# Optimization experiments

Measured on AMD Instinct MI355X. Metric: run time of the kernel, lower is better.

Reference implementation:

```python
import jax, jax.numpy as jnp
import numpy as np

D, P, R, K = 1024, 256, 64, 1024  # directions, sampling points, rank, subcarriers

def setup_inputs() -> dict:
    key = jax.random.key(0)
    k1, k2, k3 = jax.random.split(key, 3)
    return {
        "attenuation_vectors": jax.random.normal(k1, (D, P, R), dtype=jnp.float32),
        "radiation_vectors": jax.random.normal(k2, (D, P, R), dtype=jnp.float32),
        "frequency_basis_vectors": jax.random.normal(k3, (K, R), dtype=jnp.float32),
    }

def reference(attenuation_vectors, radiation_vectors, frequency_basis_vectors):
    # Original (per ray d, per subcarrier k):
    #   atten_factor[d,k] = sum_p sum_r u_rho[d,p,r] * F[k,r]
    #   rad_factor[d,k]   = sum_p sum_r u_s[d,p,r]   * F[k,r]
    #   csi[k] = (1/D) * sum_d atten_factor[d,k] * rad_factor[d,k]
    # Vectorized as two contractions over (p, r) plus a reduction over d.
    A = jnp.einsum('dpr,kr->dk', attenuation_vectors, frequency_basis_vectors)
    B = jnp.einsum('dpr,kr->dk', radiation_vectors, frequency_basis_vectors)
    num_directions = attenuation_vectors.shape[0]
    csi = jnp.sum(A * B, axis=0) / num_directions  # [K]
    return csi
```

## Files before the change

kernel.cpp:

```cpp
#include <hip/hip_runtime.h>

#define D_DIRS 1024
#define P_PTS  256
#define R_RANK 64
#define K_SUB  1024

typedef float v4f __attribute__((ext_vector_type(4)));

#define WS_A 0
#define WS_B (D_DIRS * R_RANK)
#define WS_M (2 * D_DIRS * R_RANK)
#define WS_MSUM 0
#define NB_B 32
#define DCHUNK (D_DIRS / NB_B)

__device__ __forceinline__ v4f ntload(const v4f* __restrict__ p) {
    return __builtin_nontemporal_load(p);
}

__device__ __forceinline__ v4f shfl_xor_v4(v4f v, int m) {
    v4f r;
    r.x = __shfl_xor(v.x, m);
    r.y = __shfl_xor(v.y, m);
    r.z = __shfl_xor(v.z, m);
    r.w = __shfl_xor(v.w, m);
    return r;
}

__global__ __launch_bounds__(512) void k_reduce_p(const float* __restrict__ atten,
                                                  const float* __restrict__ rad,
                                                  float* __restrict__ ws) {
    const int t    = threadIdx.x;
    const int wave = t >> 6;
    const int lane = t & 63;
    const int d    = blockIdx.x * 4 + (wave >> 1);
    const int half = wave & 1;
    const int r4g  = lane & 7;
    const int pr   = lane >> 3;

    const int base = pr * 16 + half * 8 + r4g;
    const v4f* A4 = (const v4f*)atten + (size_t)d * 4096 + base;
    const v4f* B4 = (const v4f*)rad   + (size_t)d * 4096 + base;

    v4f pa[8], pb[8], na[8], nb[8];
#pragma unroll
    for (int j = 0; j < 8; ++j) pa[j] = ntload(A4 + j * 128);
#pragma unroll
    for (int j = 0; j < 8; ++j) pb[j] = ntload(B4 + j * 128);

    v4f acc_a = {0.f, 0.f, 0.f, 0.f};
    v4f acc_b = {0.f, 0.f, 0.f, 0.f};

#pragma unroll
    for (int mc = 0; mc < 4; ++mc) {
        if (mc < 3) {
            const int off = (mc + 1) * 8 * 128;
#pragma unroll
            for (int j = 0; j < 8; ++j) na[j] = ntload(A4 + off + j * 128);
#pragma unroll
            for (int j = 0; j < 8; ++j) nb[j] = ntload(B4 + off + j * 128);
        }
        acc_a = acc_a + (((pa[0] + pa[1]) + (pa[2] + pa[3])) +
                         ((pa[4] + pa[5]) + (pa[6] + pa[7])));
        acc_b = acc_b + (((pb[0] + pb[1]) + (pb[2] + pb[3])) +
                         ((pb[4] + pb[5]) + (pb[6] + pb[7])));
#pragma unroll
        for (int j = 0; j < 8; ++j) { pa[j] = na[j]; pb[j] = nb[j]; }
    }

    acc_a = acc_a + shfl_xor_v4(acc_a, 8);
    acc_a = acc_a + shfl_xor_v4(acc_a, 16);
    acc_a = acc_a + shfl_xor_v4(acc_a, 32);
    acc_b = acc_b + shfl_xor_v4(acc_b, 8);
    acc_b = acc_b + shfl_xor_v4(acc_b, 16);
    acc_b = acc_b + shfl_xor_v4(acc_b, 32);

    if (pr == 0) {
        ((v4f*)(ws + WS_A))[d * 16 + half * 8 + r4g] = acc_a;
        ((v4f*)(ws + WS_B))[d * 16 + half * 8 + r4g] = acc_b;
    }
}

__global__ __launch_bounds__(256) void k_partial_m(float* __restrict__ ws) {
    const int bb = blockIdx.x;
    const int t  = threadIdx.x;

    __shared__ float sa[DCHUNK * R_RANK];
    __shared__ float sb[DCHUNK * R_RANK];

    const float4* a4 = (const float4*)(ws + WS_A) + bb * (DCHUNK * R_RANK / 4);
    const float4* b4 = (const float4*)(ws + WS_B) + bb * (DCHUNK * R_RANK / 4);
    float4* sa4 = (float4*)sa;
    float4* sb4 = (float4*)sb;
    sa4[t]       = a4[t];
    sa4[t + 256] = a4[t + 256];
    sb4[t]       = b4[t];
    sb4[t + 256] = b4[t + 256];
    __syncthreads();

    const int c  = t & 63;
    const int wg = t >> 6;

    float acc[16];
#pragma unroll
    for (int i = 0; i < 16; ++i) acc[i] = 0.f;

    for (int dd = 0; dd < DCHUNK; ++dd) {
        const float bv = sb[dd * 64 + c];
        const float4* ar = (const float4*)&sa[dd * 64 + wg * 16];
        const float4 a0 = ar[0], a1 = ar[1], a2 = ar[2], a3 = ar[3];
        acc[0]  += a0.x * bv; acc[1]  += a0.y * bv; acc[2]  += a0.z * bv; acc[3]  += a0.w * bv;
        acc[4]  += a1.x * bv; acc[5]  += a1.y * bv; acc[6]  += a1.z * bv; acc[7]  += a1.w * bv;
        acc[8]  += a2.x * bv; acc[9]  += a2.y * bv; acc[10] += a2.z * bv; acc[11] += a2.w * bv;
        acc[12] += a3.x * bv; acc[13] += a3.y * bv; acc[14] += a3.z * bv; acc[15] += a3.w * bv;
    }

    float* Mp = ws + WS_M + bb * 4096;
#pragma unroll
    for (int i = 0; i < 16; ++i) Mp[(wg * 16 + i) * 64 + c] = acc[i];
}

__global__ __launch_bounds__(256) void k_reduce_m(float* __restrict__ ws) {
    const int tg = blockIdx.x * 256 + threadIdx.x;
    const float4* Mp4 = (const float4*)(ws + WS_M);
    float4 s = make_float4(0.f, 0.f, 0.f, 0.f);
#pragma unroll
    for (int g = 0; g < NB_B; ++g) {
        const float4 v = Mp4[g * 1024 + tg];
        s.x += v.x; s.y += v.y; s.z += v.z; s.w += v.w;
    }
    ((float4*)(ws + WS_MSUM))[tg] = s;
}

__global__ __launch_bounds__(256) void k_csi(const float* __restrict__ ws,
                                             const float* __restrict__ freq,
                                             float* __restrict__ out) {
    const int bb = blockIdx.x;
    const int t  = threadIdx.x;

    __shared__ float Ms[64 * 68];
    __shared__ float Fs[64 * 65];
    __shared__ float red[4][64];

    const float4* M4 = (const float4*)(ws + WS_MSUM);
#pragma unroll
    for (int i = 0; i < 4; ++i) {
        const int idx4 = i * 256 + t;
        const float4 s = M4[idx4];
        const int r = idx4 >> 4, c4 = idx4 & 15;
        *(float4*)&Ms[r * 68 + c4 * 4] = s;
    }

    const float4* F4 = (const float4*)freq + bb * 1024;
#pragma unroll
    for (int i = 0; i < 4; ++i) {
        const int idx4 = i * 256 + t;
        const float4 v = F4[idx4];
        const int row = idx4 >> 4, c4 = idx4 & 15;
        Fs[row * 65 + c4 * 4 + 0] = v.x;
        Fs[row * 65 + c4 * 4 + 1] = v.y;
        Fs[row * 65 + c4 * 4 + 2] = v.z;
        Fs[row * 65 + c4 * 4 + 3] = v.w;
    }
    __syncthreads();

    const int kl = t & 63;
    const int jg = t >> 6;

    float h[16];
#pragma unroll
    for (int j = 0; j < 16; ++j) h[j] = 0.f;

    for (int r = 0; r < 64; ++r) {
        const float fv = Fs[kl * 65 + r];
        const float4* mr = (const float4*)&Ms[r * 68 + jg * 16];
        const float4 m0 = mr[0], m1 = mr[1], m2 = mr[2], m3 = mr[3];
        h[0]  += fv * m0.x; h[1]  += fv * m0.y; h[2]  += fv * m0.z; h[3]  += fv * m0.w;
        h[4]  += fv * m1.x; h[5]  += fv * m1.y; h[6]  += fv * m1.z; h[7]  += fv * m1.w;
        h[8]  += fv * m2.x; h[9]  += fv * m2.y; h[10] += fv * m2.z; h[11] += fv * m2.w;
        h[12] += fv * m3.x; h[13] += fv * m3.y; h[14] += fv * m3.z; h[15] += fv * m3.w;
    }

    float part = 0.f;
#pragma unroll
    for (int j = 0; j < 16; ++j) part += h[j] * Fs[kl * 65 + jg * 16 + j];

    red[jg][kl] = part;
    __syncthreads();
    if (t < 64) {
        out[bb * 64 + t] =
            (red[0][t] + red[1][t] + red[2][t] + red[3][t]) * (1.0f / (float)D_DIRS);
    }
}

extern "C" void kernel_launch(void* const* d_in, const int* in_sizes, int n_in,
                              void* d_out, int out_size, void* d_ws, size_t ws_size,
                              hipStream_t stream) {
    const float* atten = (const float*)d_in[0];
    const float* rad   = (const float*)d_in[1];
    const float* freq  = (const float*)d_in[2];
    float* out = (float*)d_out;
    float* ws  = (float*)d_ws;

    k_reduce_p<<<D_DIRS / 4, 512, 0, stream>>>(atten, rad, ws);
    k_partial_m<<<NB_B, 256, 0, stream>>>(ws);
    k_reduce_m<<<4, 256, 0, stream>>>(ws);
    k_csi<<<16, 256, 0, stream>>>(ws, freq, out);
}
```

Baseline: 149.4 us.

## Stream p-reduction inputs through LDS with async global_load_lds double buffering

The first kernel now reads attenuation and radiation data straight into LDS using global_load_lds, double-buffered across 16 chunks with manual waitcnt, instead of nontemporal register loads. Each wave now covers a contiguous half of the P dimension, so the per-direction partial sums are split into two halves in the workspace. The next kernel adds those halves together while staging its data into LDS. The aim is to raise the number of loads in flight and cut register pressure in this HBM-bound reduction. In exchange it adds LDS traffic and relies on hand-coded waitcnt values being correct.

```diff
diff --git a/kernel.cpp b/kernel.cpp
--- a/kernel.cpp
+++ b/kernel.cpp
@@ -1,4 +1,5 @@
 #include <hip/hip_runtime.h>
+#include <stdint.h>
 
 #define D_DIRS 1024
 #define P_PTS  256
@@ -7,16 +8,12 @@
 
 typedef float v4f __attribute__((ext_vector_type(4)));
 
-#define WS_A 0
-#define WS_B (D_DIRS * R_RANK)
-#define WS_M (2 * D_DIRS * R_RANK)
+#define WS_AP 0
+#define WS_BP (D_DIRS * 2 * R_RANK)
+#define WS_M  (2 * D_DIRS * 2 * R_RANK)
 #define WS_MSUM 0
 #define NB_B 32
 #define DCHUNK (D_DIRS / NB_B)
-
-__device__ __forceinline__ v4f ntload(const v4f* __restrict__ p) {
-    return __builtin_nontemporal_load(p);
-}
 
 __device__ __forceinline__ v4f shfl_xor_v4(v4f v, int m) {
     v4f r;
@@ -25,6 +22,12 @@
     r.z = __shfl_xor(v.z, m);
     r.w = __shfl_xor(v.w, m);
     return r;
+}
+
+__device__ __forceinline__ void load_lds_1k(const void* g, void* l) {
+    __builtin_amdgcn_global_load_lds(
+        (const __attribute__((address_space(1))) uint32_t*)g,
+        (__attribute__((address_space(3))) uint32_t*)l, 16, 0, 0);
 }
 
 __global__ __launch_bounds__(512) void k_reduce_p(const float* __restrict__ atten,
@@ -35,49 +38,58 @@
     const int lane = t & 63;
     const int d    = blockIdx.x * 4 + (wave >> 1);
     const int half = wave & 1;
-    const int r4g  = lane & 7;
-    const int pr   = lane >> 3;
-
-    const int base = pr * 16 + half * 8 + r4g;
-    const v4f* A4 = (const v4f*)atten + (size_t)d * 4096 + base;
-    const v4f* B4 = (const v4f*)rad   + (size_t)d * 4096 + base;
-
-    v4f pa[8], pb[8], na[8], nb[8];
-#pragma unroll
-    for (int j = 0; j < 8; ++j) pa[j] = ntload(A4 + j * 128);
-#pragma unroll
-    for (int j = 0; j < 8; ++j) pb[j] = ntload(B4 + j * 128);
+    const int rq   = lane & 15;
+    const int pg   = lane >> 4;
+
+    __shared__ char lds[8][2][2][2048];
+
+    const char* gA = (const char*)(atten + (size_t)d * 16384 + half * 8192);
+    const char* gB = (const char*)(rad   + (size_t)d * 16384 + half * 8192);
+    const int lane16 = lane * 16;
+
+    auto issue = [&](int c, int s) {
+        const char* ga = gA + c * 2048 + lane16;
+        const char* gb = gB + c * 2048 + lane16;
+        load_lds_1k(ga,        &lds[wave][0][s][0]);
+        load_lds_1k(ga + 1024, &lds[wave][0][s][1024]);
+        load_lds_1k(gb,        &lds[wave][1][s][0]);
+        load_lds_1k(gb + 1024, &lds[wave][1][s][1024]);
+    };
 
     v4f acc_a = {0.f, 0.f, 0.f, 0.f};
     v4f acc_b = {0.f, 0.f, 0.f, 0.f};
 
-#pragma unroll
-    for (int mc = 0; mc < 4; ++mc) {
-        if (mc < 3) {
-            const int off = (mc + 1) * 8 * 128;
-#pragma unroll
-            for (int j = 0; j < 8; ++j) na[j] = ntload(A4 + off + j * 128);
-#pragma unroll
-            for (int j = 0; j < 8; ++j) nb[j] = ntload(B4 + off + j * 128);
-        }
-        acc_a = acc_a + (((pa[0] + pa[1]) + (pa[2] + pa[3])) +
-                         ((pa[4] + pa[5]) + (pa[6] + pa[7])));
-        acc_b = acc_b + (((pb[0] + pb[1]) + (pb[2] + pb[3])) +
-                         ((pb[4] + pb[5]) + (pb[6] + pb[7])));
-#pragma unroll
-        for (int j = 0; j < 8; ++j) { pa[j] = na[j]; pb[j] = nb[j]; }
-    }
-
-    acc_a = acc_a + shfl_xor_v4(acc_a, 8);
+    auto consume = [&](int s) {
+        asm volatile("" ::: "memory");
+        const float* bufA = (const float*)&lds[wave][0][s][0];
+        const float* bufB = (const float*)&lds[wave][1][s][0];
+        const v4f a0 = *(const v4f*)(bufA + pg * 64 + rq * 4);
+        const v4f a1 = *(const v4f*)(bufA + (pg + 4) * 64 + rq * 4);
+        const v4f b0 = *(const v4f*)(bufB + pg * 64 + rq * 4);
+        const v4f b1 = *(const v4f*)(bufB + (pg + 4) * 64 + rq * 4);
+        acc_a = acc_a + (a0 + a1);
+        acc_b = acc_b + (b0 + b1);
+        asm volatile("" ::: "memory");
+    };
+
+    issue(0, 0);
+#pragma unroll
+    for (int c = 0; c < 15; ++c) {
+        issue(c + 1, (c + 1) & 1);
+        __builtin_amdgcn_s_waitcnt(0x0F74);
+        consume(c & 1);
+    }
+    __builtin_amdgcn_s_waitcnt(0x0F70);
+    consume(15 & 1);
+
     acc_a = acc_a + shfl_xor_v4(acc_a, 16);
     acc_a = acc_a + shfl_xor_v4(acc_a, 32);
-    acc_b = acc_b + shfl_xor_v4(acc_b, 8);
     acc_b = acc_b + shfl_xor_v4(acc_b, 16);
     acc_b = acc_b + shfl_xor_v4(acc_b, 32);
 
-    if (pr == 0) {
-        ((v4f*)(ws + WS_A))[d * 16 + half * 8 + r4g] = acc_a;
-        ((v4f*)(ws + WS_B))[d * 16 + half * 8 + r4g] = acc_b;
+    if (pg == 0) {
+        ((v4f*)(ws + WS_AP))[d * 32 + half * 16 + rq] = acc_a;
+        ((v4f*)(ws + WS_BP))[d * 32 + half * 16 + rq] = acc_b;
     }
 }
 
@@ -88,14 +100,18 @@
     __shared__ float sa[DCHUNK * R_RANK];
     __shared__ float sb[DCHUNK * R_RANK];
 
-    const float4* a4 = (const float4*)(ws + WS_A) + bb * (DCHUNK * R_RANK / 4);
-    const float4* b4 = (const float4*)(ws + WS_B) + bb * (DCHUNK * R_RANK / 4);
+    const float4* aP = (const float4*)(ws + WS_AP) + bb * (DCHUNK * 32);
+    const float4* bP = (const float4*)(ws + WS_BP) + bb * (DCHUNK * 32);
     float4* sa4 = (float4*)sa;
     float4* sb4 = (float4*)sb;
-    sa4[t]       = a4[t];
-    sa4[t + 256] = a4[t + 256];
-    sb4[t]       = b4[t];
-    sb4[t + 256] = b4[t + 256];
+#pragma unroll
+    for (int i = t; i < DCHUNK * 16; i += 256) {
+        const int dd = i >> 4, q = i & 15;
+        const float4 xa = aP[dd * 32 + q], ya = aP[dd * 32 + 16 + q];
+        sa4[i] = make_float4(xa.x + ya.x, xa.y + ya.y, xa.z + ya.z, xa.w + ya.w);
+        const float4 xb = bP[dd * 32 + q], yb = bP[dd * 32 + 16 + q];
+        sb4[i] = make_float4(xb.x + yb.x, xb.y + yb.y, xb.z + yb.z, xb.w + yb.w);
+    }
     __syncthreads();
 
     const int c  = t & 63;
```

New measurement: 158.6 us. 6.1% more time.
